# Kernel optimization log

Hardware: AMD Instinct MI355X
Metric: run time of the kernel (lower is better)

The kernel has to match this reference:

```python
import jax, jax.numpy as jnp
import numpy as np

H, NHEADS, DK, DV, DFF, MAXLEN = 128, 2, 96, 96, 2048, 43
VIN, VOUT = 32000, 10000
N, T = 256, 43


def layer_norm(x, g, b, eps=1e-5):
    m = jnp.mean(x, axis=-1, keepdims=True)
    v = jnp.mean(jnp.square(x - m), axis=-1, keepdims=True)
    return (x - m) / jnp.sqrt(v + eps) * g + b


def setup_inputs() -> dict:
    key = jax.random.key(0)
    ks = jax.random.split(key, 24)
    def rn(k, shape, scale=0.02):
        return jax.random.normal(k, shape, dtype=jnp.float32) * scale
    return {
        "inputs": jax.random.randint(ks[0], (N, T), 0, VIN),
        "emb": rn(ks[1], (VIN, H)),
        "pos": rn(ks[2], (MAXLEN, H)),
        "Wq": rn(ks[3], (NHEADS, H, DK), 0.05),
        "bq": jnp.zeros((NHEADS, DK), jnp.float32),
        "Wk": rn(ks[4], (NHEADS, H, DK), 0.05),
        "bk": jnp.zeros((NHEADS, DK), jnp.float32),
        "Wv": rn(ks[5], (NHEADS, H, DV), 0.05),
        "bv": jnp.zeros((NHEADS, DV), jnp.float32),
        "Wo": rn(ks[6], (NHEADS * DV, H), 0.05),
        "bo": jnp.zeros((H,), jnp.float32),
        "ln1_g": jnp.ones((H,), jnp.float32),
        "ln1_b": jnp.zeros((H,), jnp.float32),
        "W1": rn(ks[7], (H, DFF), 0.05),
        "b1": jnp.zeros((DFF,), jnp.float32),
        "W2": rn(ks[8], (DFF, H), 0.05),
        "b2": jnp.zeros((H,), jnp.float32),
        "ln2_g": jnp.ones((H,), jnp.float32),
        "ln2_b": jnp.zeros((H,), jnp.float32),
        "Wout": rn(ks[9], (H, VOUT), 0.05),
        "bout": jnp.zeros((VOUT,), jnp.float32),
    }


def reference(inputs, emb, pos, Wq, bq, Wk, bk, Wv, bv, Wo, bo,
              ln1_g, ln1_b, W1, b1, W2, b2, ln2_g, ln2_b, Wout, bout):
    Tcur = inputs.shape[1]
    # embed: token + positional, (N,T,H)
    x = emb[inputs] + pos[:Tcur]
    # multi-head attention (all heads batched on axis 'a')
    q = jnp.einsum("nth,ahk->natk", x, Wq) + bq[:, None, :]
    k = jnp.einsum("nth,ahk->natk", x, Wk) + bk[:, None, :]
    v = jnp.einsum("nth,ahv->natv", x, Wv) + bv[:, None, :]
    scores = jnp.einsum("natk,nask->nats", q, k) / jnp.sqrt(jnp.float32(DK))
    # NOTE: original mask (float-embeddings != pad_idx) is a numerical no-op; omitted.
    probs = jax.nn.softmax(scores, axis=-1)
    att = jnp.einsum("nats,nasv->natv", probs, v)          # (N,A,T,DV)
    multi = att.transpose(0, 2, 1, 3).reshape(att.shape[0], Tcur, NHEADS * DV)
    attn_out = multi @ Wo + bo
    x1 = layer_norm(x + attn_out, ln1_g, ln1_b)
    # feedforward + residual + LN
    ff = jax.nn.relu(x1 @ W1 + b1) @ W2 + b2
    x2 = layer_norm(x1 + ff, ln2_g, ln2_b)
    # final vocab projection (N,T,VOUT)
    return x2 @ Wout + bout
```

## Files before the change

### kernel.cpp

```cpp
#include <hip/hip_runtime.h>
#include <hip/hip_bf16.h>

#define H 128
#define NHEADS 2
#define DK 96
#define DV 96
#define DFF 2048
#define VOUT 10000
#define VOUT_PAD 10112
#define NB 256
#define TT 43
#define NT (NB * TT)
#define MD (NHEADS * DV)
#define MDP 256
#define QKVC 640

typedef short short8v __attribute__((ext_vector_type(8)));
typedef unsigned short ushort8v __attribute__((ext_vector_type(8)));
typedef float f32x4 __attribute__((ext_vector_type(4)));

__device__ __forceinline__ unsigned short f2bf(float f) {
    unsigned b = __float_as_uint(f);
    unsigned r = b + 0x7FFFu + ((b >> 16) & 1u);
    return (unsigned short)(r >> 16);
}
__device__ __forceinline__ float bf2f(unsigned short u) {
    return __uint_as_float((unsigned)u << 16);
}

__global__ __launch_bounds__(256) void embed_kernel(
    const int* __restrict__ inputs, const float* __restrict__ emb,
    const float* __restrict__ pos, float* __restrict__ x) {
    int i = blockIdx.x * 256 + threadIdx.x;
    int h = i & (H - 1);
    int nt = i >> 7;
    int t = nt % TT;
    x[i] = emb[inputs[nt] * H + h] + pos[t * H + h];
}

__global__ __launch_bounds__(256) void wqkv_pack_kernel(
    const float* __restrict__ Wq, const float* __restrict__ bq,
    const float* __restrict__ Wk, const float* __restrict__ bk,
    const float* __restrict__ Wv, const float* __restrict__ bv,
    unsigned short* __restrict__ Wt, float* __restrict__ bias) {
    int row = blockIdx.x * 256 + threadIdx.x;
    if (row >= QKVC) return;
    unsigned short* dst = Wt + (size_t)row * H;
    if (row < 576) {
        int seg = row / 96;
        int d = row - seg * 96;
        int which = seg >> 1;
        int head = seg & 1;
        const float* W  = (which == 0) ? Wq : (which == 1) ? Wk : Wv;
        const float* bi = (which == 0) ? bq : (which == 1) ? bk : bv;
        for (int h = 0; h < H; ++h) dst[h] = f2bf(W[((size_t)head * H + h) * DK + d]);
        bias[row] = bi[head * DK + d];
    } else {
        for (int h = 0; h < H; ++h) dst[h] = 0;
        bias[row] = 0.f;
    }
}

__global__ __launch_bounds__(256) void qkv_mfma_kernel(
    const float* __restrict__ x, const unsigned short* __restrict__ Wt,
    const float* __restrict__ bias, unsigned short* __restrict__ qkvb) {
    __shared__ __align__(16) unsigned short As[128][128];
    __shared__ __align__(16) unsigned short Bt[128][128];
    int tid = threadIdx.x;
    int n0 = blockIdx.x * 128;
    int m0 = blockIdx.y * 128;
    for (int qc = tid; qc < 2048; qc += 256) {
        int row = qc >> 4, o = qc & 15;
        const float4* src = (const float4*)(x + (size_t)(m0 + row) * H + o * 8);
        float4 f0 = src[0], f1 = src[1];
        ushort8v v;
        v[0] = f2bf(f0.x); v[1] = f2bf(f0.y); v[2] = f2bf(f0.z); v[3] = f2bf(f0.w);
        v[4] = f2bf(f1.x); v[5] = f2bf(f1.y); v[6] = f2bf(f1.z); v[7] = f2bf(f1.w);
        int po = (o & 8) | ((o ^ row) & 7);
        *(ushort8v*)&As[row][po * 8] = v;
    }
    {
        const ushort8v* B8 = (const ushort8v*)(Wt + (size_t)n0 * H);
        for (int qc = tid; qc < 2048; qc += 256) {
            int row = qc >> 4, o = qc & 15;
            int po = (o & 8) | ((o ^ row) & 7);
            *(ushort8v*)&Bt[row][po * 8] = B8[qc];
        }
    }
    __syncthreads();
    int lane = tid & 63;
    int w = tid >> 6;
    int wr = w >> 1, wc = w & 1;
    int rl = lane & 15, quad = lane >> 4;
    f32x4 acc[4][4];
    #pragma unroll
    for (int i = 0; i < 4; ++i)
        #pragma unroll
        for (int j = 0; j < 4; ++j) acc[i][j] = (f32x4){0.f, 0.f, 0.f, 0.f};
    #pragma unroll
    for (int kk = 0; kk < 4; ++kk) {
        int o = kk * 4 + quad;
        short8v a[4], b[4];
        #pragma unroll
        for (int mi = 0; mi < 4; ++mi) {
            int row = wr * 64 + mi * 16 + rl;
            int po = (o & 8) | ((o ^ row) & 7);
            a[mi] = *(const short8v*)&As[row][po * 8];
        }
        #pragma unroll
        for (int ni = 0; ni < 4; ++ni) {
            int cc = wc * 64 + ni * 16 + rl;
            int po = (o & 8) | ((o ^ cc) & 7);
            b[ni] = *(const short8v*)&Bt[cc][po * 8];
        }
        #pragma unroll
        for (int mi = 0; mi < 4; ++mi)
            #pragma unroll
            for (int ni = 0; ni < 4; ++ni)
                acc[mi][ni] = __builtin_amdgcn_mfma_f32_16x16x32_bf16(
                    a[mi], b[ni], acc[mi][ni], 0, 0, 0);
    }
    #pragma unroll
    for (int ni = 0; ni < 4; ++ni) {
        int col = n0 + wc * 64 + ni * 16 + rl;
        float bv = bias[col];
        #pragma unroll
        for (int mi = 0; mi < 4; ++mi) {
            int rbase = m0 + wr * 64 + mi * 16 + quad * 4;
            #pragma unroll
            for (int r = 0; r < 4; ++r)
                qkvb[(size_t)(rbase + r) * QKVC + col] = f2bf(acc[mi][ni][r] + bv);
        }
    }
}

__global__ __launch_bounds__(256) void attn_core_kernel(
    const unsigned short* __restrict__ qkvb, unsigned short* __restrict__ multi_b) {
    int blk = blockIdx.x;
    int n = blk / NHEADS, a = blk % NHEADS;
    int tid = threadIdx.x;
    __shared__ float qs[TT][DK];
    __shared__ float ks2[TT][DK];
    __shared__ float vs[TT][DV];
    __shared__ float ss[TT][TT + 1];
    for (int i = tid; i < TT * DK; i += 256) {
        int t = i / DK, d = i - t * DK;
        size_t base = (size_t)(n * TT + t) * QKVC + a * DK;
        qs[t][d]  = bf2f(qkvb[base + d]);
        ks2[t][d] = bf2f(qkvb[base + 192 + d]);
        vs[t][d]  = bf2f(qkvb[base + 384 + d]);
    }
    __syncthreads();
    const float scale = rsqrtf((float)DK);
    for (int o = tid; o < TT * TT; o += 256) {
        int t = o / TT, s = o - t * TT;
        float acc = 0.f;
        #pragma unroll 8
        for (int d = 0; d < DK; ++d) acc += qs[t][d] * ks2[s][d];
        ss[t][s] = acc * scale;
    }
    __syncthreads();
    if (tid < TT) {
        float m = -1e30f;
        for (int s = 0; s < TT; ++s) m = fmaxf(m, ss[tid][s]);
        float sum = 0.f;
        for (int s = 0; s < TT; ++s) { float e = __expf(ss[tid][s] - m); ss[tid][s] = e; sum += e; }
        float inv = 1.0f / sum;
        for (int s = 0; s < TT; ++s) ss[tid][s] *= inv;
    }
    __syncthreads();
    for (int o = tid; o < TT * DV; o += 256) {
        int t = o / DV, d = o - t * DV;
        float acc = 0.f;
        #pragma unroll 8
        for (int s = 0; s < TT; ++s) acc += ss[t][s] * vs[s][d];
        multi_b[(size_t)(n * TT + t) * MDP + a * DV + d] = f2bf(acc);
    }
}

__global__ __launch_bounds__(256) void wopad_kernel(
    const float* __restrict__ Wo, float* __restrict__ Wop) {
    int i = blockIdx.x * 256 + threadIdx.x;
    int row = i >> 7, col = i & 127;
    Wop[i] = (row < MD) ? Wo[row * H + col] : 0.f;
}

__global__ __launch_bounds__(256) void woln1_mfma_kernel(
    const unsigned short* __restrict__ mb, const float* __restrict__ Wop,
    const float* __restrict__ bo, const float* __restrict__ x,
    const float* __restrict__ g, const float* __restrict__ bln,
    float* __restrict__ x1) {
    __shared__ __align__(16) unsigned short As[128][128];
    __shared__ __align__(16) unsigned short Bt[128][128];
    int tid = threadIdx.x;
    int m0 = blockIdx.x * 128;
    int lane = tid & 63;
    int w = tid >> 6;
    int wr = w >> 1, wc = w & 1;
    int rl = lane & 15, quad = lane >> 4;
    f32x4 acc[4][4];
    #pragma unroll
    for (int i = 0; i < 4; ++i)
        #pragma unroll
        for (int j = 0; j < 4; ++j) acc[i][j] = (f32x4){0.f, 0.f, 0.f, 0.f};
    for (int kc = 0; kc < 2; ++kc) {
        for (int qc = tid; qc < 2048; qc += 256) {
            int row = qc >> 4, o = qc & 15;
            ushort8v v = *(const ushort8v*)(mb + (size_t)(m0 + row) * MDP + kc * 128 + o * 8);
            int po = (o & 8) | ((o ^ row) & 7);
            *(ushort8v*)&As[row][po * 8] = v;
        }
        {
            int c = tid & 127;
            int kb = tid >> 7;
            #pragma unroll
            for (int p = 0; p < 8; ++p) {
                int o = kb + 2 * p;
                ushort8v v;
                #pragma unroll
                for (int j = 0; j < 8; ++j)
                    v[j] = f2bf(Wop[(size_t)(kc * 128 + o * 8 + j) * H + c]);
                int po = (o & 8) | ((o ^ c) & 7);
                *(ushort8v*)&Bt[c][po * 8] = v;
            }
        }
        __syncthreads();
        #pragma unroll
        for (int kk = 0; kk < 4; ++kk) {
            int o = kk * 4 + quad;
            short8v a[4], b[4];
            #pragma unroll
            for (int mi = 0; mi < 4; ++mi) {
                int row = wr * 64 + mi * 16 + rl;
                int po = (o & 8) | ((o ^ row) & 7);
                a[mi] = *(const short8v*)&As[row][po * 8];
            }
            #pragma unroll
            for (int ni = 0; ni < 4; ++ni) {
                int cc = wc * 64 + ni * 16 + rl;
                int po = (o & 8) | ((o ^ cc) & 7);
                b[ni] = *(const short8v*)&Bt[cc][po * 8];
            }
            #pragma unroll
            for (int mi = 0; mi < 4; ++mi)
                #pragma unroll
                for (int ni = 0; ni < 4; ++ni)
                    acc[mi][ni] = __builtin_amdgcn_mfma_f32_16x16x32_bf16(
                        a[mi], b[ni], acc[mi][ni], 0, 0, 0);
        }
        __syncthreads();
    }
    float gg[4], bb[4], bov[4];
    #pragma unroll
    for (int ni = 0; ni < 4; ++ni) {
        int col = wc * 64 + ni * 16 + rl;
        gg[ni] = g[col]; bb[ni] = bln[col]; bov[ni] = bo[col];
    }
    float sy[4][4], sy2[4][4];
    #pragma unroll
    for (int mi = 0; mi < 4; ++mi)
        #pragma unroll
        for (int r = 0; r < 4; ++r) { sy[mi][r] = 0.f; sy2[mi][r] = 0.f; }
    #pragma unroll
    for (int mi = 0; mi < 4; ++mi) {
        #pragma unroll
        for (int r = 0; r < 4; ++r) {
            int row = wr * 64 + mi * 16 + quad * 4 + r;
            #pragma unroll
            for (int ni = 0; ni < 4; ++ni) {
                int col = wc * 64 + ni * 16 + rl;
                float y = acc[mi][ni][r] + bov[ni] + x[(size_t)(m0 + row) * H + col];
                acc[mi][ni][r] = y;
                sy[mi][r] += y;
                sy2[mi][r] += y * y;
            }
        }
    }
    #pragma unroll
    for (int mi = 0; mi < 4; ++mi)
        #pragma unroll
        for (int r = 0; r < 4; ++r) {
            #pragma unroll
            for (int m = 1; m < 16; m <<= 1) {
                sy[mi][r]  += __shfl_xor(sy[mi][r],  m);
                sy2[mi][r] += __shfl_xor(sy2[mi][r], m);
            }
        }
    float* scr = (float*)&As[0][0];
    if (rl == 0) {
        #pragma unroll
        for (int mi = 0; mi < 4; ++mi)
            #pragma unroll
            for (int r = 0; r < 4; ++r) {
                int row = wr * 64 + mi * 16 + quad * 4 + r;
                scr[wc * 128 + row]       = sy[mi][r];
                scr[256 + wc * 128 + row] = sy2[mi][r];
            }
    }
    __syncthreads();
    #pragma unroll
    for (int mi = 0; mi < 4; ++mi) {
        #pragma unroll
        for (int r = 0; r < 4; ++r) {
            int row = wr * 64 + mi * 16 + quad * 4 + r;
            float tsy  = scr[row] + scr[128 + row];
            float tsy2 = scr[256 + row] + scr[384 + row];
            float mean = tsy * (1.0f / H);
            float var  = tsy2 * (1.0f / H) - mean * mean;
            float rstd = rsqrtf(var + 1e-5f);
            #pragma unroll
            for (int ni = 0; ni < 4; ++ni) {
                int col = wc * 64 + ni * 16 + rl;
                x1[(size_t)(m0 + row) * H + col] =
                    (acc[mi][ni][r] - mean) * rstd * gg[ni] + bb[ni];
            }
        }
    }
}

__global__ __launch_bounds__(256) void ffh_kernel(
    const float* __restrict__ x1, const float* __restrict__ W1,
    const float* __restrict__ b1, unsigned short* __restrict__ hb) {
    __shared__ __align__(16) unsigned short As[128][128];
    __shared__ __align__(16) unsigned short Bt[128][128];
    int tid = threadIdx.x;
    int n0 = blockIdx.x * 128;
    int m0 = blockIdx.y * 128;
    for (int qc = tid; qc < 2048; qc += 256) {
        int row = qc >> 4, o = qc & 15;
        const float4* src = (const float4*)(x1 + (size_t)(m0 + row) * H + o * 8);
        float4 f0 = src[0], f1 = src[1];
        ushort8v v;
        v[0] = f2bf(f0.x); v[1] = f2bf(f0.y); v[2] = f2bf(f0.z); v[3] = f2bf(f0.w);
        v[4] = f2bf(f1.x); v[5] = f2bf(f1.y); v[6] = f2bf(f1.z); v[7] = f2bf(f1.w);
        int po = (o & 8) | ((o ^ row) & 7);
        *(ushort8v*)&As[row][po * 8] = v;
    }
    {
        int c = tid & 127;
        int kb = tid >> 7;
        #pragma unroll
        for (int p = 0; p < 8; ++p) {
            int o = kb + 2 * p;
            ushort8v v;
            #pragma unroll
            for (int j = 0; j < 8; ++j)
                v[j] = f2bf(W1[(size_t)(o * 8 + j) * DFF + n0 + c]);
            int po = (o & 8) | ((o ^ c) & 7);
            *(ushort8v*)&Bt[c][po * 8] = v;
        }
    }
    __syncthreads();
    int lane = tid & 63;
    int w = tid >> 6;
    int wr = w >> 1, wc = w & 1;
    int rl = lane & 15, quad = lane >> 4;
    f32x4 acc[4][4];
    #pragma unroll
    for (int i = 0; i < 4; ++i)
        #pragma unroll
        for (int j = 0; j < 4; ++j) acc[i][j] = (f32x4){0.f, 0.f, 0.f, 0.f};
    #pragma unroll
    for (int kk = 0; kk < 4; ++kk) {
        int o = kk * 4 + quad;
        short8v a[4], b[4];
        #pragma unroll
        for (int mi = 0; mi < 4; ++mi) {
            int row = wr * 64 + mi * 16 + rl;
            int po = (o & 8) | ((o ^ row) & 7);
            a[mi] = *(const short8v*)&As[row][po * 8];
        }
        #pragma unroll
        for (int ni = 0; ni < 4; ++ni) {
            int cc = wc * 64 + ni * 16 + rl;
            int po = (o & 8) | ((o ^ cc) & 7);
            b[ni] = *(const short8v*)&Bt[cc][po * 8];
        }
        #pragma unroll
        for (int mi = 0; mi < 4; ++mi)
            #pragma unroll
            for (int ni = 0; ni < 4; ++ni)
                acc[mi][ni] = __builtin_amdgcn_mfma_f32_16x16x32_bf16(
                    a[mi], b[ni], acc[mi][ni], 0, 0, 0);
    }
    #pragma unroll
    for (int ni = 0; ni < 4; ++ni) {
        int col = n0 + wc * 64 + ni * 16 + rl;
        float bv = b1[col];
        #pragma unroll
        for (int mi = 0; mi < 4; ++mi) {
            int rbase = m0 + wr * 64 + mi * 16 + quad * 4;
            #pragma unroll
            for (int r = 0; r < 4; ++r)
                hb[(size_t)(rbase + r) * DFF + col] =
                    f2bf(fmaxf(acc[mi][ni][r] + bv, 0.f));
        }
    }
}

__global__ __launch_bounds__(256) void ff2_ln2_kernel(
    const unsigned short* __restrict__ hb, const float* __restrict__ W2,
    const float* __restrict__ b2, const float* __restrict__ x1,
    const float* __restrict__ g, const float* __restrict__ bln,
    unsigned short* __restrict__ x2b) {
    __shared__ __align__(16) unsigned short As[128][128];
    __shared__ __align__(16) unsigned short Bt[128][128];
    int tid = threadIdx.x;
    int m0 = blockIdx.x * 128;
    int lane = tid & 63;
    int w = tid >> 6;
    int wr = w >> 1, wc = w & 1;
    int rl = lane & 15, quad = lane >> 4;
    f32x4 acc[4][4];
    #pragma unroll
    for (int i = 0; i < 4; ++i)
        #pragma unroll
        for (int j = 0; j < 4; ++j) acc[i][j] = (f32x4){0.f, 0.f, 0.f, 0.f};
    for (int kc = 0; kc < 16; ++kc) {
        for (int qc = tid; qc < 2048; qc += 256) {
            int row = qc >> 4, o = qc & 15;
            ushort8v v = *(const ushort8v*)(hb + (size_t)(m0 + row) * DFF + kc * 128 + o * 8);
            int po = (o & 8) | ((o ^ row) & 7);
            *(ushort8v*)&As[row][po * 8] = v;
        }
        {
            int c = tid & 127;
            int kb = tid >> 7;
            #pragma unroll
            for (int p = 0; p < 8; ++p) {
                int o = kb + 2 * p;
                ushort8v v;
                #pragma unroll
                for (int j = 0; j < 8; ++j)
                    v[j] = f2bf(W2[(size_t)(kc * 128 + o * 8 + j) * H + c]);
                int po = (o & 8) | ((o ^ c) & 7);
                *(ushort8v*)&Bt[c][po * 8] = v;
            }
        }
        __syncthreads();
        #pragma unroll
        for (int kk = 0; kk < 4; ++kk) {
            int o = kk * 4 + quad;
            short8v a[4], b[4];
            #pragma unroll
            for (int mi = 0; mi < 4; ++mi) {
                int row = wr * 64 + mi * 16 + rl;
                int po = (o & 8) | ((o ^ row) & 7);
                a[mi] = *(const short8v*)&As[row][po * 8];
            }
            #pragma unroll
            for (int ni = 0; ni < 4; ++ni) {
                int cc = wc * 64 + ni * 16 + rl;
                int po = (o & 8) | ((o ^ cc) & 7);
                b[ni] = *(const short8v*)&Bt[cc][po * 8];
            }
            #pragma unroll
            for (int mi = 0; mi < 4; ++mi)
                #pragma unroll
                for (int ni = 0; ni < 4; ++ni)
                    acc[mi][ni] = __builtin_amdgcn_mfma_f32_16x16x32_bf16(
                        a[mi], b[ni], acc[mi][ni], 0, 0, 0);
        }
        __syncthreads();
    }
    float gg[4], bb[4], bov[4];
    #pragma unroll
    for (int ni = 0; ni < 4; ++ni) {
        int col = wc * 64 + ni * 16 + rl;
        gg[ni] = g[col]; bb[ni] = bln[col]; bov[ni] = b2[col];
    }
    float sy[4][4], sy2[4][4];
    #pragma unroll
    for (int mi = 0; mi < 4; ++mi)
        #pragma unroll
        for (int r = 0; r < 4; ++r) { sy[mi][r] = 0.f; sy2[mi][r] = 0.f; }
    #pragma unroll
    for (int mi = 0; mi < 4; ++mi) {
        #pragma unroll
        for (int r = 0; r < 4; ++r) {
            int row = wr * 64 + mi * 16 + quad * 4 + r;
            #pragma unroll
            for (int ni = 0; ni < 4; ++ni) {
                int col = wc * 64 + ni * 16 + rl;
                float y = acc[mi][ni][r] + bov[ni] + x1[(size_t)(m0 + row) * H + col];
                acc[mi][ni][r] = y;
                sy[mi][r] += y;
                sy2[mi][r] += y * y;
            }
        }
    }
    #pragma unroll
    for (int mi = 0; mi < 4; ++mi)
        #pragma unroll
        for (int r = 0; r < 4; ++r) {
            #pragma unroll
            for (int m = 1; m < 16; m <<= 1) {
                sy[mi][r]  += __shfl_xor(sy[mi][r],  m);
                sy2[mi][r] += __shfl_xor(sy2[mi][r], m);
            }
        }
    float* scr = (float*)&As[0][0];
    if (rl == 0) {
        #pragma unroll
        for (int mi = 0; mi < 4; ++mi)
            #pragma unroll
            for (int r = 0; r < 4; ++r) {
                int row = wr * 64 + mi * 16 + quad * 4 + r;
                scr[wc * 128 + row]       = sy[mi][r];
                scr[256 + wc * 128 + row] = sy2[mi][r];
            }
    }
    __syncthreads();
    #pragma unroll
    for (int mi = 0; mi < 4; ++mi) {
        #pragma unroll
        for (int r = 0; r < 4; ++r) {
            int row = wr * 64 + mi * 16 + quad * 4 + r;
            float tsy  = scr[row] + scr[128 + row];
            float tsy2 = scr[256 + row] + scr[384 + row];
            float mean = tsy * (1.0f / H);
            float var  = tsy2 * (1.0f / H) - mean * mean;
            float rstd = rsqrtf(var + 1e-5f);
            #pragma unroll
            for (int ni = 0; ni < 4; ++ni) {
                int col = wc * 64 + ni * 16 + rl;
                x2b[(size_t)(m0 + row) * H + col] =
                    f2bf((acc[mi][ni][r] - mean) * rstd * gg[ni] + bb[ni]);
            }
        }
    }
}

__global__ __launch_bounds__(256) void wtr_kernel(
    const float* __restrict__ W, unsigned short* __restrict__ Wt) {
    int n = blockIdx.x * 256 + threadIdx.x;
    if (n >= VOUT_PAD) return;
    ushort8v* dst = (ushort8v*)(Wt + (size_t)n * H);
    if (n < VOUT) {
        #pragma unroll
        for (int k16 = 0; k16 < 16; ++k16) {
            ushort8v v;
            #pragma unroll
            for (int j = 0; j < 8; ++j)
                v[j] = f2bf(W[(size_t)(k16 * 8 + j) * VOUT + n]);
            dst[k16] = v;
        }
    } else {
        ushort8v z = {};
        #pragma unroll
        for (int k16 = 0; k16 < 16; ++k16) dst[k16] = z;
    }
}

__global__ __launch_bounds__(256) void out_gemm_mfma_kernel(
    const unsigned short* __restrict__ A, const unsigned short* __restrict__ Wt,
    const float* __restrict__ bias, float* __restrict__ C) {
    __shared__ __align__(16) unsigned short As[128][128];
    __shared__ __align__(16) unsigned short Bt[128][128];
    int tid = threadIdx.x;
    int n0 = blockIdx.x * 128;
    int m0 = blockIdx.y * 128;
    {
        const ushort8v* A8 = (const ushort8v*)(A + (size_t)m0 * H);
        for (int qc = tid; qc < 2048; qc += 256) {
            int row = qc >> 4, o = qc & 15;
            int po = (o & 8) | ((o ^ row) & 7);
            *(ushort8v*)&As[row][po * 8] = A8[qc];
        }
    }
    {
        const ushort8v* B8 = (const ushort8v*)(Wt + (size_t)n0 * H);
        for (int qc = tid; qc < 2048; qc += 256) {
            int row = qc >> 4, o = qc & 15;
            int po = (o & 8) | ((o ^ row) & 7);
            *(ushort8v*)&Bt[row][po * 8] = B8[qc];
        }
    }
    __syncthreads();
    int lane = tid & 63;
    int w = tid >> 6;
    int wr = w >> 1, wc = w & 1;
    int rl = lane & 15, quad = lane >> 4;
    f32x4 acc[4][4];
    #pragma unroll
    for (int i = 0; i < 4; ++i)
        #pragma unroll
        for (int j = 0; j < 4; ++j) acc[i][j] = (f32x4){0.f, 0.f, 0.f, 0.f};
    #pragma unroll
    for (int kk = 0; kk < 4; ++kk) {
        int o = kk * 4 + quad;
        short8v a[4], b[4];
        #pragma unroll
        for (int mi = 0; mi < 4; ++mi) {
            int row = wr * 64 + mi * 16 + rl;
            int po = (o & 8) | ((o ^ row) & 7);
            a[mi] = *(const short8v*)&As[row][po * 8];
        }
        #pragma unroll
        for (int ni = 0; ni < 4; ++ni) {
            int cc = wc * 64 + ni * 16 + rl;
            int po = (o & 8) | ((o ^ cc) & 7);
            b[ni] = *(const short8v*)&Bt[cc][po * 8];
        }
        #pragma unroll
        for (int mi = 0; mi < 4; ++mi)
            #pragma unroll
            for (int ni = 0; ni < 4; ++ni)
                acc[mi][ni] = __builtin_amdgcn_mfma_f32_16x16x32_bf16(
                    a[mi], b[ni], acc[mi][ni], 0, 0, 0);
    }
    #pragma unroll
    for (int ni = 0; ni < 4; ++ni) {
        int col = n0 + wc * 64 + ni * 16 + rl;
        if (col >= VOUT) continue;
        float bv = bias[col];
        #pragma unroll
        for (int mi = 0; mi < 4; ++mi) {
            int rbase = m0 + wr * 64 + mi * 16 + quad * 4;
            #pragma unroll
            for (int r = 0; r < 4; ++r)
                C[(size_t)(rbase + r) * VOUT + col] = acc[mi][ni][r] + bv;
        }
    }
}

extern "C" void kernel_launch(void* const* d_in, const int* in_sizes, int n_in,
                              void* d_out, int out_size, void* d_ws, size_t ws_size,
                              hipStream_t stream) {
    const int*   inputs = (const int*)  d_in[0];
    const float* emb    = (const float*)d_in[1];
    const float* pos    = (const float*)d_in[2];
    const float* Wq     = (const float*)d_in[3];
    const float* bq     = (const float*)d_in[4];
    const float* Wk     = (const float*)d_in[5];
    const float* bk     = (const float*)d_in[6];
    const float* Wv     = (const float*)d_in[7];
    const float* bv     = (const float*)d_in[8];
    const float* Wo     = (const float*)d_in[9];
    const float* bo     = (const float*)d_in[10];
    const float* ln1g   = (const float*)d_in[11];
    const float* ln1b   = (const float*)d_in[12];
    const float* W1     = (const float*)d_in[13];
    const float* b1     = (const float*)d_in[14];
    const float* W2     = (const float*)d_in[15];
    const float* b2     = (const float*)d_in[16];
    const float* ln2g   = (const float*)d_in[17];
    const float* ln2b   = (const float*)d_in[18];
    const float* Wout   = (const float*)d_in[19];
    const float* bout   = (const float*)d_in[20];
    float* out = (float*)d_out;

    float* ws = (float*)d_ws;
    float* x      = ws;
    float* x1     = x + (size_t)NT * H;
    float* Wo_pad = x1 + (size_t)NT * H;
    float* bqkv   = Wo_pad + (size_t)MDP * H;
    unsigned short* multi_b = (unsigned short*)(bqkv + QKVC);
    unsigned short* x2b     = multi_b + (size_t)NT * MDP;
    unsigned short* Woutb   = x2b + (size_t)NT * H;
    unsigned short* Wqkvb   = Woutb + (size_t)VOUT_PAD * H;
    unsigned short* qkvb    = Wqkvb + (size_t)QKVC * H;
    unsigned short* hb      = qkvb + (size_t)NT * QKVC;

    wqkv_pack_kernel<<<(QKVC + 255) / 256, 256, 0, stream>>>(
        Wq, bq, Wk, bk, Wv, bv, Wqkvb, bqkv);
    wopad_kernel<<<MDP * H / 256, 256, 0, stream>>>(Wo, Wo_pad);
    wtr_kernel<<<(VOUT_PAD + 255) / 256, 256, 0, stream>>>(Wout, Woutb);
    embed_kernel<<<NT * H / 256, 256, 0, stream>>>(inputs, emb, pos, x);
    dim3 gqkv(QKVC / 128, NT / 128);
    qkv_mfma_kernel<<<gqkv, 256, 0, stream>>>(x, Wqkvb, bqkv, qkvb);
    attn_core_kernel<<<NB * NHEADS, 256, 0, stream>>>(qkvb, multi_b);
    woln1_mfma_kernel<<<NT / 128, 256, 0, stream>>>(multi_b, Wo_pad, bo, x, ln1g, ln1b, x1);
    dim3 gff(DFF / 128, NT / 128);
    ffh_kernel<<<gff, 256, 0, stream>>>(x1, W1, b1, hb);
    ff2_ln2_kernel<<<NT / 128, 256, 0, stream>>>(hb, W2, b2, x1, ln2g, ln2b, x2b);
    dim3 g5((VOUT + 127) / 128, NT / 128);
    out_gemm_mfma_kernel<<<g5, 256, 0, stream>>>(x2b, Woutb, bout, out);
}
```

Baseline: 784.9 us.

## Pre-transpose weights to bf16 once and reuse bf16 activations across GEMMs

```diff
diff --git a/kernel.cpp b/kernel.cpp
--- a/kernel.cpp
+++ b/kernel.cpp
@@ -30,12 +30,15 @@
 
 __global__ __launch_bounds__(256) void embed_kernel(
     const int* __restrict__ inputs, const float* __restrict__ emb,
-    const float* __restrict__ pos, float* __restrict__ x) {
+    const float* __restrict__ pos, float* __restrict__ x,
+    unsigned short* __restrict__ xb) {
     int i = blockIdx.x * 256 + threadIdx.x;
     int h = i & (H - 1);
     int nt = i >> 7;
     int t = nt % TT;
-    x[i] = emb[inputs[nt] * H + h] + pos[t * H + h];
+    float v = emb[inputs[nt] * H + h] + pos[t * H + h];
+    x[i] = v;
+    xb[i] = f2bf(v);
 }
 
 __global__ __launch_bounds__(256) void wqkv_pack_kernel(
@@ -61,23 +64,50 @@
     }
 }
 
+__global__ __launch_bounds__(256) void w1t_kernel(
+    const float* __restrict__ W1, unsigned short* __restrict__ W1tb) {
+    int n = blockIdx.x * 256 + threadIdx.x;
+    ushort8v* dst = (ushort8v*)(W1tb + (size_t)n * H);
+    #pragma unroll
+    for (int k16 = 0; k16 < 16; ++k16) {
+        ushort8v v;
+        #pragma unroll
+        for (int j = 0; j < 8; ++j)
+            v[j] = f2bf(W1[(size_t)(k16 * 8 + j) * DFF + n]);
+        dst[k16] = v;
+    }
+}
+
+__global__ __launch_bounds__(256) void w2t_kernel(
+    const float* __restrict__ W2, unsigned short* __restrict__ W2tb) {
+    int c = blockIdx.x;
+    int j = threadIdx.x;
+    for (int k = j; k < DFF; k += 256)
+        W2tb[(size_t)c * DFF + k] = f2bf(W2[(size_t)k * H + c]);
+}
+
+__global__ __launch_bounds__(256) void wotb_kernel(
+    const float* __restrict__ Wo, unsigned short* __restrict__ Wot) {
+    int idx = blockIdx.x * 256 + threadIdx.x;
+    int c = idx >> 8, k = idx & 255;
+    Wot[(size_t)c * MDP + k] = (k < MD) ? f2bf(Wo[(size_t)k * H + c]) : (unsigned short)0;
+}
+
 __global__ __launch_bounds__(256) void qkv_mfma_kernel(
-    const float* __restrict__ x, const unsigned short* __restrict__ Wt,
+    const unsigned short* __restrict__ xb, const unsigned short* __restrict__ Wt,
     const float* __restrict__ bias, unsigned short* __restrict__ qkvb) {
     __shared__ __align__(16) unsigned short As[128][128];
     __shared__ __align__(16) unsigned short Bt[128][128];
     int tid = threadIdx.x;
     int n0 = blockIdx.x * 128;
     int m0 = blockIdx.y * 128;
-    for (int qc = tid; qc < 2048; qc += 256) {
-        int row = qc >> 4, o = qc & 15;
-        const float4* src = (const float4*)(x + (size_t)(m0 + row) * H + o * 8);
-        float4 f0 = src[0], f1 = src[1];
-        ushort8v v;
-        v[0] = f2bf(f0.x); v[1] = f2bf(f0.y); v[2] = f2bf(f0.z); v[3] = f2bf(f0.w);
-        v[4] = f2bf(f1.x); v[5] = f2bf(f1.y); v[6] = f2bf(f1.z); v[7] = f2bf(f1.w);
-        int po = (o & 8) | ((o ^ row) & 7);
-        *(ushort8v*)&As[row][po * 8] = v;
+    {
+        const ushort8v* A8 = (const ushort8v*)(xb + (size_t)m0 * H);
+        for (int qc = tid; qc < 2048; qc += 256) {
+            int row = qc >> 4, o = qc & 15;
+            int po = (o & 8) | ((o ^ row) & 7);
+            *(ushort8v*)&As[row][po * 8] = A8[qc];
+        }
     }
     {
         const ushort8v* B8 = (const ushort8v*)(Wt + (size_t)n0 * H);
@@ -143,12 +173,15 @@
     __shared__ float ks2[TT][DK];
     __shared__ float vs[TT][DV];
     __shared__ float ss[TT][TT + 1];
-    for (int i = tid; i < TT * DK; i += 256) {
-        int t = i / DK, d = i - t * DK;
-        size_t base = (size_t)(n * TT + t) * QKVC + a * DK;
-        qs[t][d]  = bf2f(qkvb[base + d]);
-        ks2[t][d] = bf2f(qkvb[base + 192 + d]);
-        vs[t][d]  = bf2f(qkvb[base + 384 + d]);
+    for (int i = tid; i < TT * 12 * 3; i += 256) {
+        int which = i / (TT * 12);
+        int rem = i - which * (TT * 12);
+        int t = rem / 12, c8 = rem - t * 12;
+        ushort8v u = *(const ushort8v*)(qkvb + (size_t)(n * TT + t) * QKVC
+                                        + a * DK + which * 192 + c8 * 8);
+        float* dst = ((which == 0) ? &qs[t][0] : (which == 1) ? &ks2[t][0] : &vs[t][0]) + c8 * 8;
+        #pragma unroll
+        for (int j = 0; j < 8; ++j) dst[j] = bf2f(u[j]);
     }
     __syncthreads();
     const float scale = rsqrtf((float)DK);
@@ -178,18 +211,11 @@
     }
 }
 
-__global__ __launch_bounds__(256) void wopad_kernel(
-    const float* __restrict__ Wo, float* __restrict__ Wop) {
-    int i = blockIdx.x * 256 + threadIdx.x;
-    int row = i >> 7, col = i & 127;
-    Wop[i] = (row < MD) ? Wo[row * H + col] : 0.f;
-}
-
 __global__ __launch_bounds__(256) void woln1_mfma_kernel(
-    const unsigned short* __restrict__ mb, const float* __restrict__ Wop,
+    const unsigned short* __restrict__ mb, const unsigned short* __restrict__ Wot,
     const float* __restrict__ bo, const float* __restrict__ x,
     const float* __restrict__ g, const float* __restrict__ bln,
-    float* __restrict__ x1) {
+    float* __restrict__ x1, unsigned short* __restrict__ x1b) {
     __shared__ __align__(16) unsigned short As[128][128];
     __shared__ __align__(16) unsigned short Bt[128][128];
     int tid = threadIdx.x;
@@ -210,19 +236,11 @@
             int po = (o & 8) | ((o ^ row) & 7);
             *(ushort8v*)&As[row][po * 8] = v;
         }
-        {
-            int c = tid & 127;
-            int kb = tid >> 7;
-            #pragma unroll
-            for (int p = 0; p < 8; ++p) {
-                int o = kb + 2 * p;
-                ushort8v v;
-                #pragma unroll
-                for (int j = 0; j < 8; ++j)
-                    v[j] = f2bf(Wop[(size_t)(kc * 128 + o * 8 + j) * H + c]);
-                int po = (o & 8) | ((o ^ c) & 7);
-                *(ushort8v*)&Bt[c][po * 8] = v;
-            }
+        for (int qc = tid; qc < 2048; qc += 256) {
+            int row = qc >> 4, o = qc & 15;
+            ushort8v v = *(const ushort8v*)(Wot + (size_t)row * MDP + kc * 128 + o * 8);
+            int po = (o & 8) | ((o ^ row) & 7);
+            *(ushort8v*)&Bt[row][po * 8] = v;
         }
         __syncthreads();
         #pragma unroll
@@ -311,43 +329,37 @@
             #pragma unroll
             for (int ni = 0; ni < 4; ++ni) {
                 int col = wc * 64 + ni * 16 + rl;
-                x1[(size_t)(m0 + row) * H + col] =
-                    (acc[mi][ni][r] - mean) * rstd * gg[ni] + bb[ni];
+                float v = (acc[mi][ni][r] - mean) * rstd * gg[ni] + bb[ni];
+                size_t idx = (size_t)(m0 + row) * H + col;
+                x1[idx] = v;
+                x1b[idx] = f2bf(v);
             }
         }
     }
 }
 
 __global__ __launch_bounds__(256) void ffh_kernel(
-    const float* __restrict__ x1, const float* __restrict__ W1,
+    const unsigned short* __restrict__ x1b, const unsigned short* __restrict__ W1tb,
     const float* __restrict__ b1, unsigned short* __restrict__ hb) {
     __shared__ __align__(16) unsigned short As[128][128];
     __shared__ __align__(16) unsigned short Bt[128][128];
     int tid = threadIdx.x;
     int n0 = blockIdx.x * 128;
     int m0 = blockIdx.y * 128;
-    for (int qc = tid; qc < 2048; qc += 256) {
-        int row = qc >> 4, o = qc & 15;
-        const float4* src = (const float4*)(x1 + (size_t)(m0 + row) * H + o * 8);
-        float4 f0 = src[0], f1 = src[1];
-        ushort8v v;
-        v[0] = f2bf(f0.x); v[1] = f2bf(f0.y); v[2] = f2bf(f0.z); v[3] = f2bf(f0.w);
-        v[4] = f2bf(f1.x); v[5] = f2bf(f1.y); v[6] = f2bf(f1.z); v[7] = f2bf(f1.w);
-        int po = (o & 8) | ((o ^ row) & 7);
-        *(ushort8v*)&As[row][po * 8] = v;
-    }
     {
-        int c = tid & 127;
-        int kb = tid >> 7;
-        #pragma unroll
-        for (int p = 0; p < 8; ++p) {
-            int o = kb + 2 * p;
-            ushort8v v;
-            #pragma unroll
-            for (int j = 0; j < 8; ++j)
-                v[j] = f2bf(W1[(size_t)(o * 8 + j) * DFF + n0 + c]);
-            int po = (o & 8) | ((o ^ c) & 7);
-            *(ushort8v*)&Bt[c][po * 8] = v;
+        const ushort8v* A8 = (const ushort8v*)(x1b + (size_t)m0 * H);
+        for (int qc = tid; qc < 2048; qc += 256) {
+            int row = qc >> 4, o = qc & 15;
+            int po = (o & 8) | ((o ^ row) & 7);
+            *(ushort8v*)&As[row][po * 8] = A8[qc];
+        }
+    }
+    {
+        const ushort8v* B8 = (const ushort8v*)(W1tb + (size_t)n0 * H);
+        for (int qc = tid; qc < 2048; qc += 256) {
+            int row = qc >> 4, o = qc & 15;
+            int po = (o & 8) | ((o ^ row) & 7);
+            *(ushort8v*)&Bt[row][po * 8] = B8[qc];
         }
     }
     __syncthreads();
@@ -399,7 +411,7 @@
 }
 
 __global__ __launch_bounds__(256) void ff2_ln2_kernel(
-    const unsigned short* __restrict__ hb, const float* __restrict__ W2,
+    const unsigned short* __restrict__ hb, const unsigned short* __restrict__ W2tb,
     const float* __restrict__ b2, const float* __restrict__ x1,
     const float* __restrict__ g, const float* __restrict__ bln,
     unsigned short* __restrict__ x2b) {
@@ -423,19 +435,11 @@
             int po = (o & 8) | ((o ^ row) & 7);
             *(ushort8v*)&As[row][po * 8] = v;
         }
-        {
-            int c = tid & 127;
-            int kb = tid >> 7;
-            #pragma unroll
-            for (int p = 0; p < 8; ++p) {
-                int o = kb + 2 * p;
-                ushort8v v;
-                #pragma unroll
-                for (int j = 0; j < 8; ++j)
-                    v[j] = f2bf(W2[(size_t)(kc * 128 + o * 8 + j) * H + c]);
-                int po = (o & 8) | ((o ^ c) & 7);
-                *(ushort8v*)&Bt[c][po * 8] = v;
-            }
+        for (int qc = tid; qc < 2048; qc += 256) {
+            int row = qc >> 4, o = qc & 15;
+            ushort8v v = *(const ushort8v*)(W2tb + (size_t)row * DFF + kc * 128 + o * 8);
+            int po = (o & 8) | ((o ^ row) & 7);
+            *(ushort8v*)&Bt[row][po * 8] = v;
         }
         __syncthreads();
         #pragma unroll
@@ -559,67 +563,75 @@
     __shared__ __align__(16) unsigned short Bt[128][128];
     int tid = threadIdx.x;
     int n0 = blockIdx.x * 128;
-    int m0 = blockIdx.y * 128;
-    {
-        const ushort8v* A8 = (const ushort8v*)(A + (size_t)m0 * H);
-        for (int qc = tid; qc < 2048; qc += 256) {
-            int row = qc >> 4, o = qc & 15;
-            int po = (o & 8) | ((o ^ row) & 7);
-            *(ushort8v*)&As[row][po * 8] = A8[qc];
-        }
-    }
-    {
-        const ushort8v* B8 = (const ushort8v*)(Wt + (size_t)n0 * H);
-        for (int qc = tid; qc < 2048; qc += 256) {
-            int row = qc >> 4, o = qc & 15;
-            int po = (o & 8) | ((o ^ row) & 7);
-            *(ushort8v*)&Bt[row][po * 8] = B8[qc];
-        }
-    }
-    __syncthreads();
     int lane = tid & 63;
     int w = tid >> 6;
     int wr = w >> 1, wc = w & 1;
     int rl = lane & 15, quad = lane >> 4;
-    f32x4 acc[4][4];
-    #pragma unroll
-    for (int i = 0; i < 4; ++i)
-        #pragma unroll
-        for (int j = 0; j < 4; ++j) acc[i][j] = (f32x4){0.f, 0.f, 0.f, 0.f};
-    #pragma unroll
-    for (int kk = 0; kk < 4; ++kk) {
-        int o = kk * 4 + quad;
-        short8v a[4], b[4];
-        #pragma unroll
-        for (int mi = 0; mi < 4; ++mi) {
-            int row = wr * 64 + mi * 16 + rl;
-            int po = (o & 8) | ((o ^ row) & 7);
-            a[mi] = *(const short8v*)&As[row][po * 8];
-        }
-        #pragma unroll
-        for (int ni = 0; ni < 4; ++ni) {
-            int cc = wc * 64 + ni * 16 + rl;
-            int po = (o & 8) | ((o ^ cc) & 7);
-            b[ni] = *(const short8v*)&Bt[cc][po * 8];
-        }
-        #pragma unroll
-        for (int mi = 0; mi < 4; ++mi)
-            #pragma unroll
-            for (int ni = 0; ni < 4; ++ni)
-                acc[mi][ni] = __builtin_amdgcn_mfma_f32_16x16x32_bf16(
-                    a[mi], b[ni], acc[mi][ni], 0, 0, 0);
-    }
+    {
+        const ushort8v* B8 = (const ushort8v*)(Wt + (size_t)n0 * H);
+        for (int qc = tid; qc < 2048; qc += 256) {
+            int row = qc >> 4, o = qc & 15;
+            int po = (o & 8) | ((o ^ row) & 7);
+            *(ushort8v*)&Bt[row][po * 8] = B8[qc];
+        }
+    }
+    float bv[4];
     #pragma unroll
     for (int ni = 0; ni < 4; ++ni) {
         int col = n0 + wc * 64 + ni * 16 + rl;
-        if (col >= VOUT) continue;
-        float bv = bias[col];
-        #pragma unroll
-        for (int mi = 0; mi < 4; ++mi) {
-            int rbase = m0 + wr * 64 + mi * 16 + quad * 4;
-            #pragma unroll
-            for (int r = 0; r < 4; ++r)
-                C[(size_t)(rbase + r) * VOUT + col] = acc[mi][ni][r] + bv;
+        bv[ni] = (col < VOUT) ? bias[col] : 0.f;
+    }
+    for (int half = 0; half < 2; ++half) {
+        int m0 = (blockIdx.y * 2 + half) * 128;
+        {
+            const ushort8v* A8 = (const ushort8v*)(A + (size_t)m0 * H);
+            for (int qc = tid; qc < 2048; qc += 256) {
+                int row = qc >> 4, o = qc & 15;
+                int po = (o & 8) | ((o ^ row) & 7);
+                *(ushort8v*)&As[row][po * 8] = A8[qc];
+            }
+        }
+        __syncthreads();
+        f32x4 acc[4][4];
+        #pragma unroll
+        for (int i = 0; i < 4; ++i)
+            #pragma unroll
+            for (int j = 0; j < 4; ++j) acc[i][j] = (f32x4){0.f, 0.f, 0.f, 0.f};
+        #pragma unroll
+        for (int kk = 0; kk < 4; ++kk) {
+            int o = kk * 4 + quad;
+            short8v a[4], b[4];
+            #pragma unroll
+            for (int mi = 0; mi < 4; ++mi) {
+                int row = wr * 64 + mi * 16 + rl;
+                int po = (o & 8) | ((o ^ row) & 7);
+                a[mi] = *(const short8v*)&As[row][po * 8];
+            }
+            #pragma unroll
+            for (int ni = 0; ni < 4; ++ni) {
+                int cc = wc * 64 + ni * 16 + rl;
+                int po = (o & 8) | ((o ^ cc) & 7);
+                b[ni] = *(const short8v*)&Bt[cc][po * 8];
+            }
+            #pragma unroll
+            for (int mi = 0; mi < 4; ++mi)
+                #pragma unroll
+                for (int ni = 0; ni < 4; ++ni)
+                    acc[mi][ni] = __builtin_amdgcn_mfma_f32_16x16x32_bf16(
+                        a[mi], b[ni], acc[mi][ni], 0, 0, 0);
+        }
+        __syncthreads();
+        #pragma unroll
+        for (int ni = 0; ni < 4; ++ni) {
+            int col = n0 + wc * 64 + ni * 16 + rl;
+            if (col >= VOUT) continue;
+            #pragma unroll
+            for (int mi = 0; mi < 4; ++mi) {
+                int rbase = m0 + wr * 64 + mi * 16 + quad * 4;
+                #pragma unroll
+                for (int r = 0; r < 4; ++r)
+                    C[(size_t)(rbase + r) * VOUT + col] = acc[mi][ni][r] + bv[ni];
+            }
         }
     }
 }
@@ -653,27 +665,33 @@
     float* ws = (float*)d_ws;
     float* x      = ws;
     float* x1     = x + (size_t)NT * H;
-    float* Wo_pad = x1 + (size_t)NT * H;
-    float* bqkv   = Wo_pad + (size_t)MDP * H;
-    unsigned short* multi_b = (unsigned short*)(bqkv + QKVC);
+    float* bqkv   = x1 + (size_t)NT * H;
+    unsigned short* xb      = (unsigned short*)(bqkv + QKVC);
+    unsigned short* x1b     = xb + (size_t)NT * H;
+    unsigned short* multi_b = x1b + (size_t)NT * H;
     unsigned short* x2b     = multi_b + (size_t)NT * MDP;
     unsigned short* Woutb   = x2b + (size_t)NT * H;
     unsigned short* Wqkvb   = Woutb + (size_t)VOUT_PAD * H;
-    unsigned short* qkvb    = Wqkvb + (size_t)QKVC * H;
+    unsigned short* W1tb    = Wqkvb + (size_t)QKVC * H;
+    unsigned short* W2tb    = W1tb + (size_t)DFF * H;
+    unsigned short* Wotb    = W2tb + (size_t)H * DFF;
+    unsigned short* qkvb    = Wotb + (size_t)H * MDP;
     unsigned short* hb      = qkvb + (size_t)NT * QKVC;
 
     wqkv_pack_kernel<<<(QKVC + 255) / 256, 256, 0, stream>>>(
         Wq, bq, Wk, bk, Wv, bv, Wqkvb, bqkv);
-    wopad_kernel<<<MDP * H / 256, 256, 0, stream>>>(Wo, Wo_pad);
+    wotb_kernel<<<H * MDP / 256, 256, 0, stream>>>(Wo, Wotb);
+    w1t_kernel<<<DFF / 256, 256, 0, stream>>>(W1, W1tb);
+    w2t_kernel<<<H, 256, 0, stream>>>(W2, W2tb);
     wtr_kernel<<<(VOUT_PAD + 255) / 256, 256, 0, stream>>>(Wout, Woutb);
-    embed_kernel<<<NT * H / 256, 256, 0, stream>>>(inputs, emb, pos, x);
+    embed_kernel<<<NT * H / 256, 256, 0, stream>>>(inputs, emb, pos, x, xb);
     dim3 gqkv(QKVC / 128, NT / 128);
-    qkv_mfma_kernel<<<gqkv, 256, 0, stream>>>(x, Wqkvb, bqkv, qkvb);
+    qkv_mfma_kernel<<<gqkv, 256, 0, stream>>>(xb, Wqkvb, bqkv, qkvb);
     attn_core_kernel<<<NB * NHEADS, 256, 0, stream>>>(qkvb, multi_b);
-    woln1_mfma_kernel<<<NT / 128, 256, 0, stream>>>(multi_b, Wo_pad, bo, x, ln1g, ln1b, x1);
+    woln1_mfma_kernel<<<NT / 128, 256, 0, stream>>>(multi_b, Wotb, bo, x, ln1g, ln1b, x1, x1b);
     dim3 gff(DFF / 128, NT / 128);
-    ffh_kernel<<<gff, 256, 0, stream>>>(x1, W1, b1, hb);
-    ff2_ln2_kernel<<<NT / 128, 256, 0, stream>>>(hb, W2, b2, x1, ln2g, ln2b, x2b);
-    dim3 g5((VOUT + 127) / 128, NT / 128);
+    ffh_kernel<<<gff, 256, 0, stream>>>(x1b, W1tb, b1, hb);
+    ff2_ln2_kernel<<<NT / 128, 256, 0, stream>>>(hb, W2tb, b2, x1, ln2g, ln2b, x2b);
+    dim3 g5(VOUT_PAD / 128, NT / 256);
     out_gemm_mfma_kernel<<<g5, 256, 0, stream>>>(x2b, Woutb, bout, out);
 }
```

After: 724.6 us. 7.7% less time.
